# Kernel optimization log

Hardware: AMD Instinct MI355X
Metric: run time of the kernel (lower is better)

Reference implementation:

```python
import jax, jax.numpy as jnp
import numpy as np

B, D, H = 16384, 1024, 1024
EPS = 1e-07


def setup_inputs() -> dict:
    key = jax.random.key(0)
    ks = jax.random.split(key, 16)
    s = 1.0 / np.sqrt(D)  # xavier-ish scale keeps exp() gate bounded
    mat = lambda k: (jax.random.normal(k, (D, H), dtype=jnp.float32) * s)
    zeros = lambda: jnp.zeros((H,), dtype=jnp.float32)
    return {
        "x": jax.random.normal(ks[0], (B, D), dtype=jnp.float32),
        "h_prev": jax.random.normal(ks[1], (B, H), dtype=jnp.float32) * 0.1,
        "c_prev": jax.random.normal(ks[2], (B, H), dtype=jnp.float32) * 0.1,
        "n_prev": jnp.ones((B, H), dtype=jnp.float32),
        "Wz": mat(ks[3]), "bWz": zeros(), "Rz": mat(ks[4]), "bRz": zeros(), "bz": zeros(),
        "Wi": mat(ks[5]), "bWi": zeros(), "Ri": mat(ks[6]), "bRi": zeros(), "bi": zeros(),
        "Wf": mat(ks[7]), "bWf": zeros(), "Rf": mat(ks[8]), "bRf": zeros(), "bf": zeros(),
        "Wo": mat(ks[9]), "bWo": zeros(), "Ro": mat(ks[10]), "bRo": zeros(), "bo": zeros(),
        "Wy": mat(ks[11]), "by": jnp.zeros((D,), dtype=jnp.float32),
    }


def reference(x, h_prev, c_prev, n_prev,
              Wz, bWz, Rz, bRz, bz,
              Wi, bWi, Ri, bRi, bi,
              Wf, bWf, Rf, bRf, bf,
              Wo, bWo, Ro, bRo, bo,
              Wy, by):
    # pre-activations: two fused GEMMs via concatenated weights
    Wcat = jnp.concatenate([Wz, Wi, Wf, Wo], axis=1)      # [D, 4H]
    Rcat = jnp.concatenate([Rz, Ri, Rf, Ro], axis=1)      # [H, 4H]
    bcat = jnp.concatenate([bWz + bRz + bz, bWi + bRi + bi,
                            bWf + bRf + bf, bWo + bRo + bo])
    pre = x @ Wcat + h_prev @ Rcat + bcat                  # [B, 4H]
    pz, pi, pf, po = jnp.split(pre, 4, axis=1)
    zt = jnp.tanh(pz)
    it = jnp.exp(pi)
    ft = jax.nn.sigmoid(pf)
    ot = jax.nn.sigmoid(po)
    C = ft * c_prev + it * zt
    n = ft * n_prev + it
    h = ot * jnp.tanh(C / (n + EPS))
    y = h @ Wy + by
    return y, (h, C, n)
```

## Files before the change

### kernel.cpp

```cpp
#include <hip/hip_runtime.h>
#include <math.h>
#include <stdint.h>


typedef __attribute__((ext_vector_type(8))) short bf16x8;
typedef __attribute__((ext_vector_type(4))) float f32x4;

constexpr int Bsz = 16384;
constexpr int Dd  = 1024;
constexpr int Hh  = 1024;
constexpr float EPSv = 1e-7f;

__device__ __forceinline__ unsigned short f2bf(float f) {
    union { float f; uint32_t u; } v; v.f = f;
    uint32_t u = v.u + 0x7fffu + ((v.u >> 16) & 1u);
    return (unsigned short)(u >> 16);
}

__device__ __forceinline__ void gload16(const void* g, void* l) {
    __builtin_amdgcn_global_load_lds(
        (const __attribute__((address_space(1))) void*)g,
        (__attribute__((address_space(3))) void*)l, 16, 0, 0);
}

__device__ __forceinline__ float sigm_f(float x) { return 1.f / (1.f + __expf(-x)); }
__device__ __forceinline__ float tanh_f(float x) {
    const float ax = fabsf(x);
    const float t = __expf(-2.f * ax);
    const float r = (1.f - t) / (1.f + t);
    return copysignf(r, x);
}

#define DSR(d, a, o) asm volatile("ds_read_b128 %0, %1 offset:" o : "=v"(d) : "v"(a) : "memory")
#define LGKM(n) { asm volatile("s_waitcnt lgkmcnt(" #n ")" ::: "memory"); __builtin_amdgcn_sched_barrier(0); }


__global__ __launch_bounds__(256)
void cvt_A(const float* __restrict__ x, const float* __restrict__ hp, unsigned short* __restrict__ A)
{
    const int idx = blockIdx.x * 256 + threadIdx.x;
    const int n = idx * 8;
    const int b = n >> 11, k = n & 2047;
    const float* s = (k < 1024) ? (x + (size_t)b * 1024 + k)
                                : (hp + (size_t)b * 1024 + (k - 1024));
    const float4 v0 = *(const float4*)s;
    const float4 v1 = *(const float4*)(s + 4);
    union { unsigned short u[8]; uint4 v; } pk;
    pk.u[0] = f2bf(v0.x); pk.u[1] = f2bf(v0.y); pk.u[2] = f2bf(v0.z); pk.u[3] = f2bf(v0.w);
    pk.u[4] = f2bf(v1.x); pk.u[5] = f2bf(v1.y); pk.u[6] = f2bf(v1.z); pk.u[7] = f2bf(v1.w);
    *(uint4*)(A + n) = pk.v;
}

struct CvtArgs {
    const float* src[9];
    const float* bptr[12];
    unsigned short* wt;
    unsigned short* wyt;
    float* bs;
};

__global__ __launch_bounds__(256)
void cvt_W(CvtArgs P)
{
    __shared__ float tile[64][65];
    const int bid = blockIdx.x;
    const int t = threadIdx.x;
    if (bid >= 2304) {
        const int j = (bid - 2304) * 256 + t;
        P.bs[j]        = P.bptr[0][j] + P.bptr[1][j]  + P.bptr[2][j];
        P.bs[1024 + j] = P.bptr[3][j] + P.bptr[4][j]  + P.bptr[5][j];
        P.bs[2048 + j] = P.bptr[6][j] + P.bptr[7][j]  + P.bptr[8][j];
        P.bs[3072 + j] = P.bptr[9][j] + P.bptr[10][j] + P.bptr[11][j];
        return;
    }
    const int id = bid >> 8, sub = bid & 255;
    const float* __restrict__ src = P.src[id];
    const int kt = sub & 15, jt = sub >> 4;
    {
        const int lr = t >> 4, lc = (t & 15) * 4;
        #pragma unroll
        for (int rr = 0; rr < 64; rr += 16) {
            const float4 v = *(const float4*)(src + (size_t)(kt * 64 + rr + lr) * 1024 + jt * 64 + lc);
            tile[rr + lr][lc + 0] = v.x;
            tile[rr + lr][lc + 1] = v.y;
            tile[rr + lr][lc + 2] = v.z;
            tile[rr + lr][lc + 3] = v.w;
        }
    }
    __syncthreads();
    const int jl = t >> 2, kc = (t & 3) * 16;
    const int j = jt * 64 + jl;
    union { unsigned short u[16]; uint4 v[2]; } pk;
    #pragma unroll
    for (int q = 0; q < 16; ++q) pk.u[q] = f2bf(tile[kc + q][jl]);
    uint4* d;
    if (id == 8) {
        d = (uint4*)(P.wyt + (size_t)j * 1024 + kt * 64 + kc);
    } else {
        const int g = id >> 1, kbase = (id & 1) ? 1024 : 0;
        const int cp = (j & 15) | (g << 4) | ((j >> 4) << 6);
        d = (uint4*)(P.wt + (size_t)cp * 2048 + kbase + kt * 64 + kc);
    }
    d[0] = pk.v[0];
    d[1] = pk.v[1];
}


template<int LD, int NTK, int NTILES, class Epi>
__device__ void mfma_core(const unsigned short* __restrict__ Ag,
                          const unsigned short* __restrict__ Bg,
                          int m0base, int n0, int t,
                          unsigned short* lds, Epi epi)
{
    constexpr int TOT = NTK * NTILES;
    const int lane = t & 63, wid = t >> 6;
    const int wr = wid >> 2, wc = wid & 3;
    const int cl = lane & 15, hi = lane >> 4;
    const int Lb = (int)(size_t)(__attribute__((address_space(3))) unsigned short*)lds;
    const int rdA0 = Lb + (wr * 128 + cl) * 128 + ((hi ^ (cl & 7)) << 4);
    const int rdB0 = Lb + 65536 + (wc * 64 + cl) * 128 + ((hi ^ (cl & 7)) << 4);
    const int srow = t >> 3;
    const int schk = ((t & 7) ^ (srow & 7)) * 8;
    const int sdst = t * 16;
    char* const L = (char*)lds;

    auto stgA = [&](int f, int buf) {
        const int ot = f / NTK, kt = f % NTK;
        const unsigned short* g = Ag + (size_t)(m0base + ot * 256 + srow) * LD + kt * 64 + schk;
        char* d = L + buf * 32768 + sdst;
        gload16(g,                  d);
        gload16(g + (size_t) 64 * LD, d + 8192);
        gload16(g + (size_t)128 * LD, d + 16384);
        gload16(g + (size_t)192 * LD, d + 24576);
    };
    auto stgB = [&](int f, int buf) {
        const int kt = f % NTK;
        const unsigned short* g = Bg + (size_t)(n0 + srow) * LD + kt * 64 + schk;
        char* d = L + 65536 + buf * 32768 + sdst;
        gload16(g,                  d);
        gload16(g + (size_t) 64 * LD, d + 8192);
        gload16(g + (size_t)128 * LD, d + 16384);
        gload16(g + (size_t)192 * LD, d + 24576);
    };

    f32x4 acc[8][4];
    #pragma unroll
    for (int i = 0; i < 8; ++i)
        #pragma unroll
        for (int j = 0; j < 4; ++j) acc[i][j] = (f32x4)0.f;

    stgA(0, 0); stgB(0, 0); stgB(1, 1);

    int bA = 0, bB = 0;
    for (int f = 0; f < TOT; ++f) {
        const int f1 = (f + 1 < TOT) ? f + 1 : TOT - 1;
        const int f2 = (f + 2 < TOT) ? f + 2 : TOT - 1;
        const int bB2 = (bB >= 1) ? bB - 1 : 2;

        asm volatile("s_waitcnt vmcnt(4)" ::: "memory");
        __builtin_amdgcn_s_barrier();
        stgA(f1, bA ^ 1);
        stgB(f2, bB2);

        const int aof  = rdA0 + (bA << 15);
        const int bof  = rdB0 + (bB << 15);
        const int aof1 = aof ^ 64;
        const int bof1 = bof ^ 64;
        bf16x8 a0[8], b0[4], a1[8], b1[4];

        DSR(b0[0], bof, "0");     DSR(b0[1], bof, "2048");
        DSR(b0[2], bof, "4096");  DSR(b0[3], bof, "6144");
        DSR(a0[0], aof, "0");     DSR(a0[1], aof, "2048");
        DSR(a0[2], aof, "4096");  DSR(a0[3], aof, "6144");
        DSR(a0[4], aof, "8192");  DSR(a0[5], aof, "10240");
        DSR(a0[6], aof, "12288"); DSR(a0[7], aof, "14336");

        LGKM(4);
        __builtin_amdgcn_s_setprio(1);
        #pragma unroll
        for (int mf = 0; mf < 4; ++mf)
            #pragma unroll
            for (int nf = 0; nf < 4; ++nf)
                acc[mf][nf] = __builtin_amdgcn_mfma_f32_16x16x32_bf16(a0[mf], b0[nf], acc[mf][nf], 0, 0, 0);
        __builtin_amdgcn_s_setprio(0);

        DSR(b1[0], bof1, "0");    DSR(b1[1], bof1, "2048");
        DSR(b1[2], bof1, "4096"); DSR(b1[3], bof1, "6144");
        DSR(a1[0], aof1, "0");    DSR(a1[1], aof1, "2048");
        DSR(a1[2], aof1, "4096"); DSR(a1[3], aof1, "6144");

        LGKM(8);
        __builtin_amdgcn_s_setprio(1);
        #pragma unroll
        for (int mf = 4; mf < 8; ++mf)
            #pragma unroll
            for (int nf = 0; nf < 4; ++nf)
                acc[mf][nf] = __builtin_amdgcn_mfma_f32_16x16x32_bf16(a0[mf], b0[nf], acc[mf][nf], 0, 0, 0);
        __builtin_amdgcn_s_setprio(0);

        DSR(a1[4], aof1, "8192");  DSR(a1[5], aof1, "10240");
        DSR(a1[6], aof1, "12288"); DSR(a1[7], aof1, "14336");

        LGKM(4);
        __builtin_amdgcn_s_setprio(1);
        #pragma unroll
        for (int mf = 0; mf < 4; ++mf)
            #pragma unroll
            for (int nf = 0; nf < 4; ++nf)
                acc[mf][nf] = __builtin_amdgcn_mfma_f32_16x16x32_bf16(a1[mf], b1[nf], acc[mf][nf], 0, 0, 0);
        __builtin_amdgcn_s_setprio(0);

        LGKM(0);
        __builtin_amdgcn_s_setprio(1);
        #pragma unroll
        for (int mf = 4; mf < 8; ++mf)
            #pragma unroll
            for (int nf = 0; nf < 4; ++nf)
                acc[mf][nf] = __builtin_amdgcn_mfma_f32_16x16x32_bf16(a1[mf], b1[nf], acc[mf][nf], 0, 0, 0);
        __builtin_amdgcn_s_setprio(0);

        if ((f % NTK) == NTK - 1) {
            epi(f / NTK, acc);
            #pragma unroll
            for (int i = 0; i < 8; ++i)
                #pragma unroll
                for (int j = 0; j < 4; ++j) acc[i][j] = (f32x4)0.f;
        }
        bA ^= 1;
        bB = (bB == 2) ? 0 : bB + 1;
    }
    asm volatile("s_waitcnt vmcnt(0)" ::: "memory");
}

__global__ __launch_bounds__(512, 2)
void gemm_gates(const unsigned short* __restrict__ A, const unsigned short* __restrict__ WT,
                const float* __restrict__ bsum,
                const float* __restrict__ c_prev, const float* __restrict__ n_prev,
                float* __restrict__ out_h, float* __restrict__ out_C, float* __restrict__ out_n,
                unsigned short* __restrict__ h_bf)
{
    __shared__ unsigned short lds[81920];
    const int t = threadIdx.x;
    const int b = blockIdx.x;
    const int nb  = (b & 7) * 2 + (b >> 7);
    const int mb0 = ((b >> 3) & 15) * 4;
    const int m0base = mb0 * 256;
    const int n0 = nb * 256;

    const int lane = t & 63, wid = t >> 6;
    const int wr = wid >> 2, wc = wid & 3;
    const int cl = lane & 15, hi = lane >> 4;
    const int j_out = nb * 64 + wc * 16 + cl;
    const float bz_ = bsum[j_out];
    const float bi_ = bsum[1024 + j_out];
    const float bf_ = bsum[2048 + j_out];
    const float bo_ = bsum[3072 + j_out];

    auto epi = [&](int ot, f32x4 (&acc)[8][4]) {
        #pragma unroll
        for (int mf = 0; mf < 8; ++mf) {
            const int rb = m0base + ot * 256 + wr * 128 + mf * 16 + hi * 4;
            #pragma unroll
            for (int r = 0; r < 4; ++r) {
                const size_t idx = (size_t)(rb + r) * 1024 + j_out;
                const float pz = acc[mf][0][r] + bz_;
                const float pi = acc[mf][1][r] + bi_;
                const float pf = acc[mf][2][r] + bf_;
                const float po = acc[mf][3][r] + bo_;
                const float zt = tanh_f(pz);
                const float it = __expf(pi);
                const float ft = sigm_f(pf);
                const float ot_ = sigm_f(po);
                const float Cv = ft * c_prev[idx] + it * zt;
                const float nv = ft * n_prev[idx] + it;
                const float hv = ot_ * tanh_f(Cv / (nv + EPSv));
                out_h[idx] = hv;
                out_C[idx] = Cv;
                out_n[idx] = nv;
                h_bf[idx] = f2bf(hv);
            }
        }
    };

    mfma_core<2048, 32, 4>(A, WT, m0base, n0, t, lds, epi);
}

__global__ __launch_bounds__(512, 2)
void gemm_y(const unsigned short* __restrict__ A, const unsigned short* __restrict__ WyT,
            const float* __restrict__ by, float* __restrict__ y)
{
    __shared__ unsigned short lds[81920];
    const int t = threadIdx.x;
    const int b = blockIdx.x;
    const int nb = b & 3, mb = b >> 2;
    const int m0base = mb * 256, n0 = nb * 256;

    const int lane = t & 63, wid = t >> 6;
    const int wr = wid >> 2, wc = wid & 3;
    const int cl = lane & 15, hi = lane >> 4;

    auto epi = [&](int ot, f32x4 (&acc)[8][4]) {
        (void)ot;
        #pragma unroll
        for (int mf = 0; mf < 8; ++mf) {
            const int rb = m0base + wr * 128 + mf * 16 + hi * 4;
            #pragma unroll
            for (int nf = 0; nf < 4; ++nf) {
                const int c = n0 + wc * 64 + nf * 16 + cl;
                const float bc = by[c];
                #pragma unroll
                for (int r = 0; r < 4; ++r)
                    y[(size_t)(rb + r) * 1024 + c] = acc[mf][nf][r] + bc;
            }
        }
    };

    mfma_core<1024, 16, 1>(A, WyT, m0base, n0, t, lds, epi);
}


constexpr int FBM = 64, FBN = 64, FBK = 16, FPAD = 4;

__global__ __launch_bounds__(256)
void fb_gates(const float* __restrict__ x, const float* __restrict__ h_prev,
              const float* __restrict__ c_prev, const float* __restrict__ n_prev,
              const float* __restrict__ Wz, const float* __restrict__ Rz,
              const float* __restrict__ Wi, const float* __restrict__ Ri,
              const float* __restrict__ Wf, const float* __restrict__ Rf,
              const float* __restrict__ Wo, const float* __restrict__ Ro,
              const float* __restrict__ bWz, const float* __restrict__ bRz, const float* __restrict__ bz,
              const float* __restrict__ bWi, const float* __restrict__ bRi, const float* __restrict__ bi,
              const float* __restrict__ bWf, const float* __restrict__ bRf, const float* __restrict__ bf_,
              const float* __restrict__ bWo, const float* __restrict__ bRo, const float* __restrict__ bo,
              float* __restrict__ out_h, float* __restrict__ out_C, float* __restrict__ out_n)
{
    __shared__ float sA[FBK][FBM + FPAD];
    __shared__ float sB[4][FBK][FBN + FPAD];
    const int t = threadIdx.x;
    const int col_blk = blockIdx.x & 15, row_blk = blockIdx.x >> 4;
    const int row0 = row_blk * FBM, col0 = col_blk * FBN;
    const int tx = t & 15, ty = t >> 4;
    float acc[4][4][4];
    #pragma unroll
    for (int g = 0; g < 4; ++g)
        for (int i = 0; i < 4; ++i)
            for (int j = 0; j < 4; ++j) acc[g][i][j] = 0.f;
    const int ar = t >> 2, ak = (t & 3) * 4, wk = t >> 4, wcc = (t & 15) * 4;
    for (int phase = 0; phase < 2; ++phase) {
        const float* Am = phase ? h_prev : x;
        const float* W0 = phase ? Rz : Wz; const float* W1 = phase ? Ri : Wi;
        const float* W2 = phase ? Rf : Wf; const float* W3 = phase ? Ro : Wo;
        for (int k0 = 0; k0 < 1024; k0 += FBK) {
            __syncthreads();
            {
                const float4 v = *(const float4*)(Am + (size_t)(row0 + ar) * 1024 + k0 + ak);
                sA[ak + 0][ar] = v.x; sA[ak + 1][ar] = v.y;
                sA[ak + 2][ar] = v.z; sA[ak + 3][ar] = v.w;
            }
            *(float4*)&sB[0][wk][wcc] = *(const float4*)(W0 + (size_t)(k0 + wk) * 1024 + col0 + wcc);
            *(float4*)&sB[1][wk][wcc] = *(const float4*)(W1 + (size_t)(k0 + wk) * 1024 + col0 + wcc);
            *(float4*)&sB[2][wk][wcc] = *(const float4*)(W2 + (size_t)(k0 + wk) * 1024 + col0 + wcc);
            *(float4*)&sB[3][wk][wcc] = *(const float4*)(W3 + (size_t)(k0 + wk) * 1024 + col0 + wcc);
            __syncthreads();
            #pragma unroll
            for (int kk = 0; kk < FBK; ++kk) {
                float a[4], bb[4][4];
                *(float4*)a = *(const float4*)&sA[kk][ty * 4];
                *(float4*)&bb[0][0] = *(const float4*)&sB[0][kk][tx * 4];
                *(float4*)&bb[1][0] = *(const float4*)&sB[1][kk][tx * 4];
                *(float4*)&bb[2][0] = *(const float4*)&sB[2][kk][tx * 4];
                *(float4*)&bb[3][0] = *(const float4*)&sB[3][kk][tx * 4];
                #pragma unroll
                for (int g = 0; g < 4; ++g)
                    for (int i = 0; i < 4; ++i)
                        for (int j = 0; j < 4; ++j)
                            acc[g][i][j] += a[i] * bb[g][j];
            }
        }
    }
    #pragma unroll
    for (int i = 0; i < 4; ++i) {
        const int r = row0 + ty * 4 + i;
        #pragma unroll
        for (int j = 0; j < 4; ++j) {
            const int c = col0 + tx * 4 + j;
            const float pz = acc[0][i][j] + bWz[c] + bRz[c] + bz[c];
            const float pi = acc[1][i][j] + bWi[c] + bRi[c] + bi[c];
            const float pf = acc[2][i][j] + bWf[c] + bRf[c] + bf_[c];
            const float po = acc[3][i][j] + bWo[c] + bRo[c] + bo[c];
            const float zt = tanhf(pz);
            const float it = expf(pi);
            const float ft = 1.f / (1.f + expf(-pf));
            const float ot = 1.f / (1.f + expf(-po));
            const size_t idx = (size_t)r * Hh + c;
            const float Cv = ft * c_prev[idx] + it * zt;
            const float nv = ft * n_prev[idx] + it;
            out_h[idx] = ot * tanhf(Cv / (nv + EPSv));
            out_C[idx] = Cv;
            out_n[idx] = nv;
        }
    }
}

__global__ __launch_bounds__(256)
void fb_ygemm(const float* __restrict__ hmat, const float* __restrict__ Wy,
              const float* __restrict__ by, float* __restrict__ y)
{
    __shared__ float sA[FBK][FBM + FPAD];
    __shared__ float sB[FBK][FBN + FPAD];
    const int t = threadIdx.x;
    const int col_blk = blockIdx.x & 15, row_blk = blockIdx.x >> 4;
    const int row0 = row_blk * FBM, col0 = col_blk * FBN;
    const int tx = t & 15, ty = t >> 4;
    float acc[4][4];
    #pragma unroll
    for (int i = 0; i < 4; ++i)
        for (int j = 0; j < 4; ++j) acc[i][j] = 0.f;
    const int ar = t >> 2, ak = (t & 3) * 4, wk = t >> 4, wcc = (t & 15) * 4;
    for (int k0 = 0; k0 < 1024; k0 += FBK) {
        __syncthreads();
        {
            const float4 v = *(const float4*)(hmat + (size_t)(row0 + ar) * 1024 + k0 + ak);
            sA[ak + 0][ar] = v.x; sA[ak + 1][ar] = v.y;
            sA[ak + 2][ar] = v.z; sA[ak + 3][ar] = v.w;
        }
        *(float4*)&sB[wk][wcc] = *(const float4*)(Wy + (size_t)(k0 + wk) * 1024 + col0 + wcc);
        __syncthreads();
        #pragma unroll
        for (int kk = 0; kk < FBK; ++kk) {
            float a[4], bb[4];
            *(float4*)a = *(const float4*)&sA[kk][ty * 4];
            *(float4*)bb = *(const float4*)&sB[kk][tx * 4];
            #pragma unroll
            for (int i = 0; i < 4; ++i)
                for (int j = 0; j < 4; ++j)
                    acc[i][j] += a[i] * bb[j];
        }
    }
    #pragma unroll
    for (int i = 0; i < 4; ++i) {
        const int r = row0 + ty * 4 + i;
        #pragma unroll
        for (int j = 0; j < 4; ++j) {
            const int c = col0 + tx * 4 + j;
            y[(size_t)r * Dd + c] = acc[i][j] + by[c];
        }
    }
}


extern "C" void kernel_launch(void* const* d_in, const int* in_sizes, int n_in,
                              void* d_out, int out_size, void* d_ws, size_t ws_size,
                              hipStream_t stream) {
    const float* x      = (const float*)d_in[0];
    const float* h_prev = (const float*)d_in[1];
    const float* c_prev = (const float*)d_in[2];
    const float* n_prev = (const float*)d_in[3];
    const float* Wz  = (const float*)d_in[4];
    const float* bWz = (const float*)d_in[5];
    const float* Rz  = (const float*)d_in[6];
    const float* bRz = (const float*)d_in[7];
    const float* bz  = (const float*)d_in[8];
    const float* Wi  = (const float*)d_in[9];
    const float* bWi = (const float*)d_in[10];
    const float* Ri  = (const float*)d_in[11];
    const float* bRi = (const float*)d_in[12];
    const float* bi  = (const float*)d_in[13];
    const float* Wf  = (const float*)d_in[14];
    const float* bWf = (const float*)d_in[15];
    const float* Rf  = (const float*)d_in[16];
    const float* bRf = (const float*)d_in[17];
    const float* bf_ = (const float*)d_in[18];
    const float* Wo  = (const float*)d_in[19];
    const float* bWo = (const float*)d_in[20];
    const float* Ro  = (const float*)d_in[21];
    const float* bRo = (const float*)d_in[22];
    const float* bo  = (const float*)d_in[23];
    const float* Wy  = (const float*)d_in[24];
    const float* by  = (const float*)d_in[25];

    float* y     = (float*)d_out;
    float* out_h = y + (size_t)Bsz * Dd;
    float* out_C = out_h + (size_t)Bsz * Hh;
    float* out_n = out_C + (size_t)Bsz * Hh;

    const size_t OFF_A    = 0;
    const size_t OFF_WT   = 67108864;
    const size_t OFF_WYT  = 83886080;
    const size_t OFF_HBF  = 85983232;
    const size_t OFF_BS   = 119537664;
    const size_t WS_NEED  = 119554048;

    if (ws_size >= WS_NEED) {
        char* ws = (char*)d_ws;
        unsigned short* A_bf = (unsigned short*)(ws + OFF_A);
        unsigned short* WT   = (unsigned short*)(ws + OFF_WT);
        unsigned short* WyT  = (unsigned short*)(ws + OFF_WYT);
        unsigned short* h_bf = (unsigned short*)(ws + OFF_HBF);
        float* bsum          = (float*)(ws + OFF_BS);

        cvt_A<<<16384, 256, 0, stream>>>(x, h_prev, A_bf);

        CvtArgs P;
        P.src[0] = Wz; P.src[1] = Rz; P.src[2] = Wi; P.src[3] = Ri;
        P.src[4] = Wf; P.src[5] = Rf; P.src[6] = Wo; P.src[7] = Ro; P.src[8] = Wy;
        P.bptr[0] = bWz; P.bptr[1] = bRz; P.bptr[2]  = bz;
        P.bptr[3] = bWi; P.bptr[4] = bRi; P.bptr[5]  = bi;
        P.bptr[6] = bWf; P.bptr[7] = bRf; P.bptr[8]  = bf_;
        P.bptr[9] = bWo; P.bptr[10] = bRo; P.bptr[11] = bo;
        P.wt = WT; P.wyt = WyT; P.bs = bsum;
        cvt_W<<<2308, 256, 0, stream>>>(P);

        gemm_gates<<<256, 512, 0, stream>>>(A_bf, WT, bsum, c_prev, n_prev,
                                            out_h, out_C, out_n, h_bf);
        gemm_y<<<256, 512, 0, stream>>>(h_bf, WyT, by, y);
    } else {
        dim3 block(256);
        dim3 grid((Bsz / FBM) * (Hh / FBN));
        fb_gates<<<grid, block, 0, stream>>>(x, h_prev, c_prev, n_prev,
                                             Wz, Rz, Wi, Ri, Wf, Rf, Wo, Ro,
                                             bWz, bRz, bz, bWi, bRi, bi,
                                             bWf, bRf, bf_, bWo, bRo, bo,
                                             out_h, out_C, out_n);
        fb_ygemm<<<grid, block, 0, stream>>>(out_h, Wy, by, y);
    }
}
```

Baseline: 428.1 us.

## Load B fragments directly from global in MFMA-packed layout, bypass LDS

The weight-prep kernel now writes the transposed weights in a fragment-packed order that matches the MFMA B operand per lane. The GEMM core then loads B straight into registers from global memory instead of staging it through LDS, and LDS shrinks to just the double-buffered A tile. This removes B's LDS traffic and ds_reads and cuts shared memory use. In exchange, each wave re-reads B from global/L2 with no sharing across waves, and the B register prefetch for the next step has less latency hiding.

```diff
diff --git a/kernel.cpp b/kernel.cpp
--- a/kernel.cpp
+++ b/kernel.cpp
@@ -33,6 +33,7 @@
 
 #define DSR(d, a, o) asm volatile("ds_read_b128 %0, %1 offset:" o : "=v"(d) : "v"(a) : "memory")
 #define LGKM(n) { asm volatile("s_waitcnt lgkmcnt(" #n ")" ::: "memory"); __builtin_amdgcn_sched_barrier(0); }
+#define VMC(n)  { asm volatile("s_waitcnt vmcnt(" #n ")" ::: "memory"); __builtin_amdgcn_sched_barrier(0); }
 
 
 __global__ __launch_bounds__(256)
@@ -93,39 +94,51 @@
     union { unsigned short u[16]; uint4 v[2]; } pk;
     #pragma unroll
     for (int q = 0; q < 16; ++q) pk.u[q] = f2bf(tile[kc + q][jl]);
-    uint4* d;
+
+    int g, cl_, NKTv, kbase;
+    unsigned short* base;
     if (id == 8) {
-        d = (uint4*)(P.wyt + (size_t)j * 1024 + kt * 64 + kc);
+        g = j >> 4; cl_ = j & 15; NKTv = 16; kbase = 0; base = P.wyt;
     } else {
-        const int g = id >> 1, kbase = (id & 1) ? 1024 : 0;
-        const int cp = (j & 15) | (g << 4) | ((j >> 4) << 6);
-        d = (uint4*)(P.wt + (size_t)cp * 2048 + kbase + kt * 64 + kc);
-    }
-    d[0] = pk.v[0];
-    d[1] = pk.v[1];
-}
-
-
-template<int LD, int NTK, int NTILES, class Epi>
+        const int gt = id >> 1;
+        const int cp = (j & 15) | (gt << 4) | ((j >> 4) << 6);
+        g = cp >> 4; cl_ = cp & 15; NKTv = 32;
+        kbase = (id & 1) ? 1024 : 0; base = P.wt;
+    }
+    const int gk = kbase + kt * 64 + kc;
+    const int KT = gk >> 6, ks = (gk >> 5) & 1, hi0 = (gk >> 3) & 3;
+    const size_t off = ((((size_t)g * NKTv + KT) * 2 + ks) * 64 + hi0 * 16 + cl_) * 8;
+    *(uint4*)(base + off)       = pk.v[0];
+    *(uint4*)(base + off + 128) = pk.v[1];
+}
+
+
+template<int LD, int NKT, int NTILES, class Epi>
 __device__ void mfma_core(const unsigned short* __restrict__ Ag,
-                          const unsigned short* __restrict__ Bg,
-                          int m0base, int n0, int t,
+                          const unsigned short* __restrict__ Bp,
+                          int m0base, int g0, int t,
                           unsigned short* lds, Epi epi)
 {
-    constexpr int TOT = NTK * NTILES;
+    constexpr int TOT = NKT * NTILES;
     const int lane = t & 63, wid = t >> 6;
     const int wr = wid >> 2, wc = wid & 3;
     const int cl = lane & 15, hi = lane >> 4;
     const int Lb = (int)(size_t)(__attribute__((address_space(3))) unsigned short*)lds;
     const int rdA0 = Lb + (wr * 128 + cl) * 128 + ((hi ^ (cl & 7)) << 4);
-    const int rdB0 = Lb + 65536 + (wc * 64 + cl) * 128 + ((hi ^ (cl & 7)) << 4);
     const int srow = t >> 3;
     const int schk = ((t & 7) ^ (srow & 7)) * 8;
     const int sdst = t * 16;
     char* const L = (char*)lds;
 
+    int bvo[8];
+    #pragma unroll
+    for (int j = 0; j < 8; ++j) {
+        const int nf = j & 3, ks = j >> 2;
+        bvo[j] = (((g0 + wc * 4 + nf) * NKT * 2) + ks) * 1024 + lane * 16;
+    }
+
     auto stgA = [&](int f, int buf) {
-        const int ot = f / NTK, kt = f % NTK;
+        const int ot = f / NKT, kt = f % NKT;
         const unsigned short* g = Ag + (size_t)(m0base + ot * 256 + srow) * LD + kt * 64 + schk;
         char* d = L + buf * 32768 + sdst;
         gload16(g,                  d);
@@ -133,14 +146,13 @@
         gload16(g + (size_t)128 * LD, d + 16384);
         gload16(g + (size_t)192 * LD, d + 24576);
     };
-    auto stgB = [&](int f, int buf) {
-        const int kt = f % NTK;
-        const unsigned short* g = Bg + (size_t)(n0 + srow) * LD + kt * 64 + schk;
-        char* d = L + 65536 + buf * 32768 + sdst;
-        gload16(g,                  d);
-        gload16(g + (size_t) 64 * LD, d + 8192);
-        gload16(g + (size_t)128 * LD, d + 16384);
-        gload16(g + (size_t)192 * LD, d + 24576);
+
+    bf16x8 b[8];
+    auto ldB = [&](int f) {
+        const int ko = (f % NKT) * 2048;
+        #pragma unroll
+        for (int j = 0; j < 8; ++j)
+            b[j] = *(const bf16x8*)((const char*)Bp + (size_t)(bvo[j] + ko));
     };
 
     f32x4 acc[8][4];
@@ -149,31 +161,27 @@
         #pragma unroll
         for (int j = 0; j < 4; ++j) acc[i][j] = (f32x4)0.f;
 
-    stgA(0, 0); stgB(0, 0); stgB(1, 1);
-
-    int bA = 0, bB = 0;
+    stgA(0, 0);
+    ldB(0);
+
     for (int f = 0; f < TOT; ++f) {
+        const int bA = f & 1;
         const int f1 = (f + 1 < TOT) ? f + 1 : TOT - 1;
-        const int f2 = (f + 2 < TOT) ? f + 2 : TOT - 1;
-        const int bB2 = (bB >= 1) ? bB - 1 : 2;
-
-        asm volatile("s_waitcnt vmcnt(4)" ::: "memory");
+
+        VMC(8);
         __builtin_amdgcn_s_barrier();
         stgA(f1, bA ^ 1);
-        stgB(f2, bB2);
 
         const int aof  = rdA0 + (bA << 15);
-        const int bof  = rdB0 + (bB << 15);
         const int aof1 = aof ^ 64;
-        const int bof1 = bof ^ 64;
-        bf16x8 a0[8], b0[4], a1[8], b1[4];
-
-        DSR(b0[0], bof, "0");     DSR(b0[1], bof, "2048");
-        DSR(b0[2], bof, "4096");  DSR(b0[3], bof, "6144");
-        DSR(a0[0], aof, "0");     DSR(a0[1], aof, "2048");
-        DSR(a0[2], aof, "4096");  DSR(a0[3], aof, "6144");
-        DSR(a0[4], aof, "8192");  DSR(a0[5], aof, "10240");
-        DSR(a0[6], aof, "12288"); DSR(a0[7], aof, "14336");
+        bf16x8 a0k0[4], a0k1[4], a1k0[4], a1k1[4];
+
+        DSR(a0k0[0], aof, "0");     DSR(a0k0[1], aof, "2048");
+        DSR(a0k0[2], aof, "4096");  DSR(a0k0[3], aof, "6144");
+        DSR(a0k1[0], aof1, "0");    DSR(a0k1[1], aof1, "2048");
+        DSR(a0k1[2], aof1, "4096"); DSR(a0k1[3], aof1, "6144");
+
+        VMC(4);
 
         LGKM(4);
         __builtin_amdgcn_s_setprio(1);
@@ -181,25 +189,22 @@
         for (int mf = 0; mf < 4; ++mf)
             #pragma unroll
             for (int nf = 0; nf < 4; ++nf)
-                acc[mf][nf] = __builtin_amdgcn_mfma_f32_16x16x32_bf16(a0[mf], b0[nf], acc[mf][nf], 0, 0, 0);
+                acc[mf][nf] = __builtin_amdgcn_mfma_f32_16x16x32_bf16(a0k0[mf], b[nf], acc[mf][nf], 0, 0, 0);
         __builtin_amdgcn_s_setprio(0);
 
-        DSR(b1[0], bof1, "0");    DSR(b1[1], bof1, "2048");
-        DSR(b1[2], bof1, "4096"); DSR(b1[3], bof1, "6144");
-        DSR(a1[0], aof1, "0");    DSR(a1[1], aof1, "2048");
-        DSR(a1[2], aof1, "4096"); DSR(a1[3], aof1, "6144");
+        DSR(a1k0[0], aof, "8192");  DSR(a1k0[1], aof, "10240");
+        DSR(a1k0[2], aof, "12288"); DSR(a1k0[3], aof, "14336");
+        DSR(a1k1[0], aof1, "8192");  DSR(a1k1[1], aof1, "10240");
+        DSR(a1k1[2], aof1, "12288"); DSR(a1k1[3], aof1, "14336");
 
         LGKM(8);
         __builtin_amdgcn_s_setprio(1);
         #pragma unroll
-        for (int mf = 4; mf < 8; ++mf)
+        for (int mf = 0; mf < 4; ++mf)
             #pragma unroll
             for (int nf = 0; nf < 4; ++nf)
-                acc[mf][nf] = __builtin_amdgcn_mfma_f32_16x16x32_bf16(a0[mf], b0[nf], acc[mf][nf], 0, 0, 0);
+                acc[mf][nf] = __builtin_amdgcn_mfma_f32_16x16x32_bf16(a0k1[mf], b[4 + nf], acc[mf][nf], 0, 0, 0);
         __builtin_amdgcn_s_setprio(0);
-
-        DSR(a1[4], aof1, "8192");  DSR(a1[5], aof1, "10240");
-        DSR(a1[6], aof1, "12288"); DSR(a1[7], aof1, "14336");
 
         LGKM(4);
         __builtin_amdgcn_s_setprio(1);
@@ -207,45 +212,45 @@
         for (int mf = 0; mf < 4; ++mf)
             #pragma unroll
             for (int nf = 0; nf < 4; ++nf)
-                acc[mf][nf] = __builtin_amdgcn_mfma_f32_16x16x32_bf16(a1[mf], b1[nf], acc[mf][nf], 0, 0, 0);
+                acc[4 + mf][nf] = __builtin_amdgcn_mfma_f32_16x16x32_bf16(a1k0[mf], b[nf], acc[4 + mf][nf], 0, 0, 0);
         __builtin_amdgcn_s_setprio(0);
 
         LGKM(0);
         __builtin_amdgcn_s_setprio(1);
         #pragma unroll
-        for (int mf = 4; mf < 8; ++mf)
+        for (int mf = 0; mf < 4; ++mf)
             #pragma unroll
             for (int nf = 0; nf < 4; ++nf)
-                acc[mf][nf] = __builtin_amdgcn_mfma_f32_16x16x32_bf16(a1[mf], b1[nf], acc[mf][nf], 0, 0, 0);
+                acc[4 + mf][nf] = __builtin_amdgcn_mfma_f32_16x16x32_bf16(a1k1[mf], b[4 + nf], acc[4 + mf][nf], 0, 0, 0);
         __builtin_amdgcn_s_setprio(0);
 
-        if ((f % NTK) == NTK - 1) {
-            epi(f / NTK, acc);
+        ldB(f1);
+
+        if ((f % NKT) == NKT - 1) {
+            epi(f / NKT, acc);
             #pragma unroll
             for (int i = 0; i < 8; ++i)
                 #pragma unroll
                 for (int j = 0; j < 4; ++j) acc[i][j] = (f32x4)0.f;
         }
-        bA ^= 1;
-        bB = (bB == 2) ? 0 : bB + 1;
     }
     asm volatile("s_waitcnt vmcnt(0)" ::: "memory");
 }
 
 __global__ __launch_bounds__(512, 2)
-void gemm_gates(const unsigned short* __restrict__ A, const unsigned short* __restrict__ WT,
+void gemm_gates(const unsigned short* __restrict__ A, const unsigned short* __restrict__ Bp,
                 const float* __restrict__ bsum,
                 const float* __restrict__ c_prev, const float* __restrict__ n_prev,
                 float* __restrict__ out_h, float* __restrict__ out_C, float* __restrict__ out_n,
                 unsigned short* __restrict__ h_bf)
 {
-    __shared__ unsigned short lds[81920];
+    __shared__ unsigned short lds[32768];
     const int t = threadIdx.x;
     const int b = blockIdx.x;
     const int nb  = (b & 7) * 2 + (b >> 7);
     const int mb0 = ((b >> 3) & 15) * 4;
     const int m0base = mb0 * 256;
-    const int n0 = nb * 256;
+    const int g0 = nb * 16;
 
     const int lane = t & 63, wid = t >> 6;
     const int wr = wid >> 2, wc = wid & 3;
@@ -282,18 +287,19 @@
         }
     };
 
-    mfma_core<2048, 32, 4>(A, WT, m0base, n0, t, lds, epi);
+    mfma_core<2048, 32, 4>(A, Bp, m0base, g0, t, lds, epi);
 }
 
 __global__ __launch_bounds__(512, 2)
-void gemm_y(const unsigned short* __restrict__ A, const unsigned short* __restrict__ WyT,
+void gemm_y(const unsigned short* __restrict__ A, const unsigned short* __restrict__ Wyp,
             const float* __restrict__ by, float* __restrict__ y)
 {
-    __shared__ unsigned short lds[81920];
+    __shared__ unsigned short lds[32768];
     const int t = threadIdx.x;
     const int b = blockIdx.x;
     const int nb = b & 3, mb = b >> 2;
-    const int m0base = mb * 256, n0 = nb * 256;
+    const int m0base = mb * 256;
+    const int g0 = nb * 16;
 
     const int lane = t & 63, wid = t >> 6;
     const int wr = wid >> 2, wc = wid & 3;
@@ -306,7 +312,7 @@
             const int rb = m0base + wr * 128 + mf * 16 + hi * 4;
             #pragma unroll
             for (int nf = 0; nf < 4; ++nf) {
-                const int c = n0 + wc * 64 + nf * 16 + cl;
+                const int c = nb * 256 + wc * 64 + nf * 16 + cl;
                 const float bc = by[c];
                 #pragma unroll
                 for (int r = 0; r < 4; ++r)
@@ -315,7 +321,7 @@
         }
     };
 
-    mfma_core<1024, 16, 1>(A, WyT, m0base, n0, t, lds, epi);
+    mfma_core<1024, 16, 1>(A, Wyp, m0base, g0, t, lds, epi);
 }
 
 
```

Result: slower. 452.7 us (+5.7%).

## Shrink GEMM block tiles to 128x128 with 4 waves and more blocks

Applied to the files above, without the earlier changes.

Both bf16 MFMA GEMMs move from 512-thread blocks with 256x256 output tiles to 256-thread blocks with 128x128 tiles and half the LDS. Each block now walks more row tiles (8 for gates, 4 for y). The gates grid doubles to 512 blocks and the N/M mapping changes to match. The aim is better occupancy and load balance across the CUs. The cost is lower arithmetic intensity per LDS byte and more global traffic for the B operand, since fewer blocks share each weight tile.

```diff
diff --git a/kernel.cpp b/kernel.cpp
--- a/kernel.cpp
+++ b/kernel.cpp
@@ -33,6 +33,7 @@
 
 #define DSR(d, a, o) asm volatile("ds_read_b128 %0, %1 offset:" o : "=v"(d) : "v"(a) : "memory")
 #define LGKM(n) { asm volatile("s_waitcnt lgkmcnt(" #n ")" ::: "memory"); __builtin_amdgcn_sched_barrier(0); }
+#define VMC(n)  { asm volatile("s_waitcnt vmcnt(" #n ")" ::: "memory"); __builtin_amdgcn_sched_barrier(0); }
 
 
 __global__ __launch_bounds__(256)
@@ -106,84 +107,73 @@
 }
 
 
-template<int LD, int NTK, int NTILES, class Epi>
+template<int LD, int NKT, int NTILES, class Epi>
 __device__ void mfma_core(const unsigned short* __restrict__ Ag,
                           const unsigned short* __restrict__ Bg,
                           int m0base, int n0, int t,
                           unsigned short* lds, Epi epi)
 {
-    constexpr int TOT = NTK * NTILES;
+    constexpr int TOT = NKT * NTILES;
     const int lane = t & 63, wid = t >> 6;
-    const int wr = wid >> 2, wc = wid & 3;
+    const int wr = wid >> 1, wc = wid & 1;
     const int cl = lane & 15, hi = lane >> 4;
     const int Lb = (int)(size_t)(__attribute__((address_space(3))) unsigned short*)lds;
-    const int rdA0 = Lb + (wr * 128 + cl) * 128 + ((hi ^ (cl & 7)) << 4);
-    const int rdB0 = Lb + 65536 + (wc * 64 + cl) * 128 + ((hi ^ (cl & 7)) << 4);
+    const int rdA0 = Lb + (wr * 64 + cl) * 128 + ((hi ^ (cl & 7)) << 4);
+    const int rdB0 = Lb + 32768 + (wc * 64 + cl) * 128 + ((hi ^ (cl & 7)) << 4);
     const int srow = t >> 3;
     const int schk = ((t & 7) ^ (srow & 7)) * 8;
     const int sdst = t * 16;
     char* const L = (char*)lds;
 
     auto stgA = [&](int f, int buf) {
-        const int ot = f / NTK, kt = f % NTK;
-        const unsigned short* g = Ag + (size_t)(m0base + ot * 256 + srow) * LD + kt * 64 + schk;
-        char* d = L + buf * 32768 + sdst;
+        const int ot = f / NKT, kt = f % NKT;
+        const unsigned short* g = Ag + (size_t)(m0base + ot * 128 + srow) * LD + kt * 64 + schk;
+        char* d = L + buf * 16384 + sdst;
         gload16(g,                  d);
-        gload16(g + (size_t) 64 * LD, d + 8192);
-        gload16(g + (size_t)128 * LD, d + 16384);
-        gload16(g + (size_t)192 * LD, d + 24576);
+        gload16(g + (size_t)32 * LD, d + 4096);
+        gload16(g + (size_t)64 * LD, d + 8192);
+        gload16(g + (size_t)96 * LD, d + 12288);
     };
     auto stgB = [&](int f, int buf) {
-        const int kt = f % NTK;
+        const int kt = f % NKT;
         const unsigned short* g = Bg + (size_t)(n0 + srow) * LD + kt * 64 + schk;
-        char* d = L + 65536 + buf * 32768 + sdst;
+        char* d = L + 32768 + buf * 16384 + sdst;
         gload16(g,                  d);
-        gload16(g + (size_t) 64 * LD, d + 8192);
-        gload16(g + (size_t)128 * LD, d + 16384);
-        gload16(g + (size_t)192 * LD, d + 24576);
+        gload16(g + (size_t)32 * LD, d + 4096);
+        gload16(g + (size_t)64 * LD, d + 8192);
+        gload16(g + (size_t)96 * LD, d + 12288);
     };
 
-    f32x4 acc[8][4];
+    f32x4 acc[4][4];
     #pragma unroll
-    for (int i = 0; i < 8; ++i)
+    for (int i = 0; i < 4; ++i)
         #pragma unroll
         for (int j = 0; j < 4; ++j) acc[i][j] = (f32x4)0.f;
 
     stgA(0, 0); stgB(0, 0); stgB(1, 1);
 
-    int bA = 0, bB = 0;
+    int bB = 0;
     for (int f = 0; f < TOT; ++f) {
+        const int bA = f & 1;
         const int f1 = (f + 1 < TOT) ? f + 1 : TOT - 1;
         const int f2 = (f + 2 < TOT) ? f + 2 : TOT - 1;
         const int bB2 = (bB >= 1) ? bB - 1 : 2;
 
-        asm volatile("s_waitcnt vmcnt(4)" ::: "memory");
+        VMC(4);
         __builtin_amdgcn_s_barrier();
         stgA(f1, bA ^ 1);
         stgB(f2, bB2);
 
-        const int aof  = rdA0 + (bA << 15);
-        const int bof  = rdB0 + (bB << 15);
+        const int aof  = rdA0 + (bA << 14);
+        const int bof  = rdB0 + bB * 16384;
         const int aof1 = aof ^ 64;
         const int bof1 = bof ^ 64;
-        bf16x8 a0[8], b0[4], a1[8], b1[4];
+        bf16x8 a0[4], b0[4], a1[4], b1[4];
 
         DSR(b0[0], bof, "0");     DSR(b0[1], bof, "2048");
         DSR(b0[2], bof, "4096");  DSR(b0[3], bof, "6144");
         DSR(a0[0], aof, "0");     DSR(a0[1], aof, "2048");
         DSR(a0[2], aof, "4096");  DSR(a0[3], aof, "6144");
-        DSR(a0[4], aof, "8192");  DSR(a0[5], aof, "10240");
-        DSR(a0[6], aof, "12288"); DSR(a0[7], aof, "14336");
-
-        LGKM(4);
-        __builtin_amdgcn_s_setprio(1);
-        #pragma unroll
-        for (int mf = 0; mf < 4; ++mf)
-            #pragma unroll
-            for (int nf = 0; nf < 4; ++nf)
-                acc[mf][nf] = __builtin_amdgcn_mfma_f32_16x16x32_bf16(a0[mf], b0[nf], acc[mf][nf], 0, 0, 0);
-        __builtin_amdgcn_s_setprio(0);
-
         DSR(b1[0], bof1, "0");    DSR(b1[1], bof1, "2048");
         DSR(b1[2], bof1, "4096"); DSR(b1[3], bof1, "6144");
         DSR(a1[0], aof1, "0");    DSR(a1[1], aof1, "2048");
@@ -192,16 +182,13 @@
         LGKM(8);
         __builtin_amdgcn_s_setprio(1);
         #pragma unroll
-        for (int mf = 4; mf < 8; ++mf)
+        for (int mf = 0; mf < 4; ++mf)
             #pragma unroll
             for (int nf = 0; nf < 4; ++nf)
                 acc[mf][nf] = __builtin_amdgcn_mfma_f32_16x16x32_bf16(a0[mf], b0[nf], acc[mf][nf], 0, 0, 0);
         __builtin_amdgcn_s_setprio(0);
 
-        DSR(a1[4], aof1, "8192");  DSR(a1[5], aof1, "10240");
-        DSR(a1[6], aof1, "12288"); DSR(a1[7], aof1, "14336");
-
-        LGKM(4);
+        LGKM(0);
         __builtin_amdgcn_s_setprio(1);
         #pragma unroll
         for (int mf = 0; mf < 4; ++mf)
@@ -210,56 +197,46 @@
                 acc[mf][nf] = __builtin_amdgcn_mfma_f32_16x16x32_bf16(a1[mf], b1[nf], acc[mf][nf], 0, 0, 0);
         __builtin_amdgcn_s_setprio(0);
 
-        LGKM(0);
-        __builtin_amdgcn_s_setprio(1);
-        #pragma unroll
-        for (int mf = 4; mf < 8; ++mf)
-            #pragma unroll
-            for (int nf = 0; nf < 4; ++nf)
-                acc[mf][nf] = __builtin_amdgcn_mfma_f32_16x16x32_bf16(a1[mf], b1[nf], acc[mf][nf], 0, 0, 0);
-        __builtin_amdgcn_s_setprio(0);
-
-        if ((f % NTK) == NTK - 1) {
-            epi(f / NTK, acc);
-            #pragma unroll
-            for (int i = 0; i < 8; ++i)
+        if ((f % NKT) == NKT - 1) {
+            epi(f / NKT, acc);
+            #pragma unroll
+            for (int i = 0; i < 4; ++i)
                 #pragma unroll
                 for (int j = 0; j < 4; ++j) acc[i][j] = (f32x4)0.f;
         }
-        bA ^= 1;
         bB = (bB == 2) ? 0 : bB + 1;
     }
     asm volatile("s_waitcnt vmcnt(0)" ::: "memory");
 }
 
-__global__ __launch_bounds__(512, 2)
+__global__ __launch_bounds__(256, 2)
 void gemm_gates(const unsigned short* __restrict__ A, const unsigned short* __restrict__ WT,
                 const float* __restrict__ bsum,
                 const float* __restrict__ c_prev, const float* __restrict__ n_prev,
                 float* __restrict__ out_h, float* __restrict__ out_C, float* __restrict__ out_n,
                 unsigned short* __restrict__ h_bf)
 {
-    __shared__ unsigned short lds[81920];
+    __shared__ unsigned short lds[40960];
     const int t = threadIdx.x;
     const int b = blockIdx.x;
-    const int nb  = (b & 7) * 2 + (b >> 7);
-    const int mb0 = ((b >> 3) & 15) * 4;
-    const int m0base = mb0 * 256;
-    const int n0 = nb * 256;
+    const int nb  = (b & 7) * 4 + (b >> 7);
+    const int mc  = (b >> 3) & 15;
+    const int m0base = mc * 1024;
+    const int n0 = nb * 128;
 
     const int lane = t & 63, wid = t >> 6;
-    const int wr = wid >> 2, wc = wid & 3;
+    const int wr = wid >> 1, wc = wid & 1;
     const int cl = lane & 15, hi = lane >> 4;
-    const int j_out = nb * 64 + wc * 16 + cl;
+    const int j_out = nb * 32 + wc * 16 + cl;
     const float bz_ = bsum[j_out];
     const float bi_ = bsum[1024 + j_out];
     const float bf_ = bsum[2048 + j_out];
     const float bo_ = bsum[3072 + j_out];
 
-    auto epi = [&](int ot, f32x4 (&acc)[8][4]) {
-        #pragma unroll
-        for (int mf = 0; mf < 8; ++mf) {
-            const int rb = m0base + ot * 256 + wr * 128 + mf * 16 + hi * 4;
+    auto epi = [&](int ot, f32x4 (&acc)[4][4]) {
+        #pragma unroll
+        for (int mf = 0; mf < 4; ++mf) {
+            const int rb = m0base + ot * 128 + wr * 64 + mf * 16 + hi * 4;
             #pragma unroll
             for (int r = 0; r < 4; ++r) {
                 const size_t idx = (size_t)(rb + r) * 1024 + j_out;
@@ -282,28 +259,28 @@
         }
     };
 
-    mfma_core<2048, 32, 4>(A, WT, m0base, n0, t, lds, epi);
-}
-
-__global__ __launch_bounds__(512, 2)
+    mfma_core<2048, 32, 8>(A, WT, m0base, n0, t, lds, epi);
+}
+
+__global__ __launch_bounds__(256, 2)
 void gemm_y(const unsigned short* __restrict__ A, const unsigned short* __restrict__ WyT,
             const float* __restrict__ by, float* __restrict__ y)
 {
-    __shared__ unsigned short lds[81920];
+    __shared__ unsigned short lds[40960];
     const int t = threadIdx.x;
     const int b = blockIdx.x;
-    const int nb = b & 3, mb = b >> 2;
-    const int m0base = mb * 256, n0 = nb * 256;
+    const int nb = b & 7, mc = b >> 3;
+    const int m0base = mc * 512;
+    const int n0 = nb * 128;
 
     const int lane = t & 63, wid = t >> 6;
-    const int wr = wid >> 2, wc = wid & 3;
+    const int wr = wid >> 1, wc = wid & 1;
     const int cl = lane & 15, hi = lane >> 4;
 
-    auto epi = [&](int ot, f32x4 (&acc)[8][4]) {
-        (void)ot;
-        #pragma unroll
-        for (int mf = 0; mf < 8; ++mf) {
-            const int rb = m0base + wr * 128 + mf * 16 + hi * 4;
+    auto epi = [&](int ot, f32x4 (&acc)[4][4]) {
+        #pragma unroll
+        for (int mf = 0; mf < 4; ++mf) {
+            const int rb = m0base + ot * 128 + wr * 64 + mf * 16 + hi * 4;
             #pragma unroll
             for (int nf = 0; nf < 4; ++nf) {
                 const int c = n0 + wc * 64 + nf * 16 + cl;
@@ -315,7 +292,7 @@
         }
     };
 
-    mfma_core<1024, 16, 1>(A, WyT, m0base, n0, t, lds, epi);
+    mfma_core<1024, 16, 4>(A, WyT, m0base, n0, t, lds, epi);
 }
 
 
@@ -511,9 +488,9 @@
         P.wt = WT; P.wyt = WyT; P.bs = bsum;
         cvt_W<<<2308, 256, 0, stream>>>(P);
 
-        gemm_gates<<<256, 512, 0, stream>>>(A_bf, WT, bsum, c_prev, n_prev,
+        gemm_gates<<<512, 256, 0, stream>>>(A_bf, WT, bsum, c_prev, n_prev,
                                             out_h, out_C, out_n, h_bf);
-        gemm_y<<<256, 512, 0, stream>>>(h_bf, WyT, by, y);
+        gemm_y<<<256, 256, 0, stream>>>(h_bf, WyT, by, y);
     } else {
         dim3 block(256);
         dim3 grid((Bsz / FBM) * (Hh / FBN));
```

New measurement: 469.6 us. 9.7% more time.
